# Performance work log

Hardware: AMD Instinct MI355X
Metric: run time of the kernel (lower is better)

Reference implementation:

```python
import jax, jax.numpy as jnp
import numpy as np

D_EMB = 1024
B, T = 8, 2048

def setup_inputs() -> dict:
    key = jax.random.key(0)
    ks = jax.random.split(key, 7)
    s = 0.02
    return {
        "x": jax.random.normal(ks[0], (B, T, D_EMB), dtype=jnp.float32),
        "W_attn": jax.random.normal(ks[1], (3 * D_EMB, D_EMB), dtype=jnp.float32) * s,
        "b_attn": jax.random.normal(ks[2], (3 * D_EMB,), dtype=jnp.float32) * s,
        "W_proj": jax.random.normal(ks[3], (D_EMB, D_EMB), dtype=jnp.float32) * s,
        "b_proj": jax.random.normal(ks[4], (D_EMB,), dtype=jnp.float32) * s,
        "W_fc": jax.random.normal(ks[5], (1, D_EMB), dtype=jnp.float32) * s,
        "b_fc": jax.random.normal(ks[6], (1,), dtype=jnp.float32) * s,
    }

def reference(x, W_attn, b_attn, W_proj, b_proj, W_fc, b_fc):
    # qkv projection: torch Linear => x @ W.T + b
    qkv = jnp.einsum('btc,dc->btd', x, W_attn) + b_attn          # [B,T,3C]
    q, k, v = jnp.split(qkv, 3, axis=2)                          # each [B,T,C]
    scale = q.shape[-1] ** (-0.5)
    attn_scores = jnp.einsum('btc,bsc->bts', q, k) * scale       # [B,T,T]
    attn_weights = jax.nn.softmax(attn_scores, axis=-1)          # traditional softmax
    y = jnp.einsum('bts,bsc->btc', attn_weights, v)              # [B,T,C]
    y = jnp.einsum('btc,dc->btd', y, W_proj) + b_proj            # [B,T,C]
    out = jnp.einsum('btc,oc->bto', y, W_fc) + b_fc              # [B,T,1]
    return out
```

## Files before the change

### kernel.cpp

```cpp
#include <hip/hip_runtime.h>
#include <stdint.h>

#define D_EMB 1024
#define NBATCH 8
#define SEQ 2048
#define MTOT (NBATCH*SEQ)

typedef __attribute__((ext_vector_type(8))) short short8;
typedef __attribute__((ext_vector_type(4))) float f32x4;

__device__ __forceinline__ ushort bf16r(float x) {
  union { float f; uint32_t u; } c; c.f = x;
  return (ushort)((c.u + 0x7fffu + ((c.u >> 16) & 1u)) >> 16);
}

__device__ __forceinline__ void cp16(const ushort* g, ushort* l) {
  __builtin_amdgcn_global_load_lds(
      (const __attribute__((address_space(1))) void*)g,
      (__attribute__((address_space(3))) void*)l, 16, 0, 0);
}

__global__ __launch_bounds__(256) void cvt_all(
    const float4* __restrict__ x4, const float4* __restrict__ W4,
    const float4* __restrict__ wv4, const float* __restrict__ sc,
    ushort* __restrict__ xb, ushort* __restrict__ wqkb, float* __restrict__ vw) {
  int tid = threadIdx.x;
  if (blockIdx.x < 4096) {
    int wave = tid >> 6, lane = tid & 63;
    long row = (long)blockIdx.x * 4 + wave;
    const float4* xr = x4 + row * 256;
    ushort* xo = xb + row * D_EMB;
    float s = 0.f;
    #pragma unroll
    for (int i = 0; i < 4; i++) {
      int idx = lane + i * 64;
      float4 v = xr[idx];
      float4 w = wv4[idx];
      *(ushort4*)(xo + idx * 4) = make_ushort4(bf16r(v.x), bf16r(v.y), bf16r(v.z), bf16r(v.w));
      s += v.x * w.x + v.y * w.y + v.z * w.z + v.w * w.w;
    }
    #pragma unroll
    for (int off = 32; off; off >>= 1) s += __shfl_xor(s, off);
    if (lane == 0) vw[row] = s + sc[1];
  } else {
    long base = (long)(blockIdx.x - 4096) * 1024 + tid;
    #pragma unroll
    for (int i = 0; i < 4; i++) {
      long idx = base + i * 256;
      float4 v = W4[idx];
      *(ushort4*)(wqkb + idx * 4) = make_ushort4(bf16r(v.x), bf16r(v.y), bf16r(v.z), bf16r(v.w));
    }
  }
}

__global__ void init_kernel(const float* __restrict__ bp, const float* __restrict__ Wfc,
                            const float* __restrict__ bfc,
                            float* __restrict__ w_eff, float* __restrict__ wv_eff,
                            float* __restrict__ numden, float* __restrict__ sc) {
  int tid = threadIdx.x;
  int b = blockIdx.x;
  if (b == 0) { w_eff[tid] = 0.f; return; }
  if (b == 1) { wv_eff[tid] = 0.f; return; }
  if (b >= 3) { numden[(long)(b - 3) * 1024 + tid] = 0.f; return; }
  float v = bp[tid] * Wfc[tid];
  int lane = tid & 63, w = tid >> 6;
  #pragma unroll
  for (int off = 32; off; off >>= 1) v += __shfl_xor(v, off);
  __shared__ float red[16];
  if (lane == 0) red[w] = v;
  __syncthreads();
  if (tid == 0) {
    float s = 0.f;
    #pragma unroll
    for (int i = 0; i < 16; i++) s += red[i];
    sc[0] = s + bfc[0];
  }
}

__global__ void prep1(const float* __restrict__ Wp, const float* __restrict__ Wfc,
                      float* __restrict__ w_eff) {
  int c = blockIdx.x * 256 + threadIdx.x;
  int d0 = blockIdx.y * 16;
  float s = 0.f;
  #pragma unroll
  for (int d = d0; d < d0 + 16; d++) s += Wfc[d] * Wp[(long)d * D_EMB + c];
  atomicAdd(&w_eff[c], s);
}

__global__ void prep2(const float* __restrict__ Wattn, const float* __restrict__ battn,
                      const float* __restrict__ w_eff, float* __restrict__ wv_eff,
                      float* __restrict__ sc) {
  int tid = threadIdx.x;
  if (blockIdx.y == 64) {
    if (blockIdx.x != 0) return;
    float v = 0.f;
    #pragma unroll
    for (int i = 0; i < 4; i++) { int c = tid + i * 256; v += battn[2048 + c] * w_eff[c]; }
    int lane = tid & 63, w = tid >> 6;
    #pragma unroll
    for (int off = 32; off; off >>= 1) v += __shfl_xor(v, off);
    __shared__ float red[4];
    if (lane == 0) red[w] = v;
    __syncthreads();
    if (tid == 0) sc[1] = red[0] + red[1] + red[2] + red[3];
    return;
  }
  int d = blockIdx.x * 256 + tid;
  int c0 = blockIdx.y * 16;
  float s = 0.f;
  #pragma unroll
  for (int c = c0; c < c0 + 16; c++) s += w_eff[c] * Wattn[(long)(2048 + c) * D_EMB + d];
  atomicAdd(&wv_eff[d], s);
}

template<bool FUSED, bool REMAP>
__global__ __launch_bounds__(512, 2) void gemm_nt(
    const ushort* __restrict__ A, long lda, long sAz,
    const ushort* __restrict__ B, long ldb, long sBz,
    ushort* __restrict__ C, long ldc,
    const float* __restrict__ bias, float scale, int K,
    const float* __restrict__ vw, float* __restrict__ num, float* __restrict__ den) {
  __shared__ __align__(16) ushort lds[65536];

  int bx, by, z;
  if (REMAP) {
    int f = (int)(blockIdx.x + 8u * blockIdx.y);
    int xcd = f & 7, g = f >> 3;
    bx = g & 7; by = xcd * 8 + (g >> 3); z = 0;
  } else {
    bx = blockIdx.x; by = blockIdx.y; z = blockIdx.z;
  }

  const ushort* Az = A + (long)z * sAz;
  const ushort* Bz = B + (long)z * sBz;
  long m0 = (long)by * 256, n0 = (long)bx * 256;
  int t = threadIdx.x;
  int wave = t >> 6, lane = t & 63;
  int r = lane & 15, q = lane >> 4;
  int wm = wave >> 2, wn = wave & 3;

  f32x4 acc[8][4] = {};

  int rl = t >> 3;
  int cs = t & 7;
  int gc = cs ^ (rl & 7);
  const ushort* pA = Az + (m0 + rl) * lda + gc * 8;
  const ushort* pB = Bz + (n0 + rl) * ldb + gc * 8;
  long a64 = 64 * lda, a128 = 128 * lda;
  long b64 = 64 * ldb, b128s = 128 * ldb;
  int dst = t * 8;

  int sw8 = (q ^ (r & 7)) * 8;
  int aoff = (wm * 128 + r) * 64 + sw8;
  int boff = (wn * 64 + r) * 64 + sw8;

  int NT = K >> 6;

#define STG_A(BUF, H, TT) do { \
    cp16(pA + (long)(TT) * 64 + (H) * a128,       lds + (BUF) * 16384 + (H) * 8192 + dst); \
    cp16(pA + (long)(TT) * 64 + (H) * a128 + a64, lds + (BUF) * 16384 + (H) * 8192 + 4096 + dst); \
  } while (0)
#define STG_B(BUF, H, TT) do { \
    cp16(pB + (long)(TT) * 64 + (H) * b128s,       lds + 32768 + (BUF) * 16384 + (H) * 8192 + dst); \
    cp16(pB + (long)(TT) * 64 + (H) * b128s + b64, lds + 32768 + (BUF) * 16384 + (H) * 8192 + 4096 + dst); \
  } while (0)

#define LDA_Q(BUF, QA) do { \
    _Pragma("unroll") \
    for (int i = 0; i < 4; i++) { \
      af[0][i] = *(const short8*)(lds + (BUF) * 16384 + ( aoff + (QA) * 4096 + i * 1024       )); \
      af[1][i] = *(const short8*)(lds + (BUF) * 16384 + ((aoff + (QA) * 4096 + i * 1024) ^ 32 )); \
    } \
  } while (0)
#define LDB_Q(BUF, QB, BF) do { \
    _Pragma("unroll") \
    for (int j = 0; j < 2; j++) { \
      BF[0][j] = *(const short8*)(lds + 32768 + (BUF) * 16384 + ( boff + (QB) * 2048 + j * 1024       )); \
      BF[1][j] = *(const short8*)(lds + 32768 + (BUF) * 16384 + ((boff + (QB) * 2048 + j * 1024) ^ 32 )); \
    } \
  } while (0)

#define MM_Q(QA, QB, BF) do { \
    __builtin_amdgcn_s_setprio(1); \
    _Pragma("unroll") \
    for (int kk = 0; kk < 2; kk++) { \
      _Pragma("unroll") \
      for (int i = 0; i < 4; i++) { \
        _Pragma("unroll") \
        for (int j = 0; j < 2; j++) \
          acc[(QA) * 4 + i][(QB) * 2 + j] = __builtin_amdgcn_mfma_f32_16x16x32_bf16( \
              af[kk][i], BF[kk][j], acc[(QA) * 4 + i][(QB) * 2 + j], 0, 0, 0); \
      } \
    } \
    __builtin_amdgcn_s_setprio(0); \
  } while (0)

#define BAR __builtin_amdgcn_s_barrier()
#define LGKM0 asm volatile("s_waitcnt lgkmcnt(0)" ::: "memory")
#define VM4 asm volatile("s_waitcnt vmcnt(4)" ::: "memory")
#define VM0 asm volatile("s_waitcnt vmcnt(0)" ::: "memory")

#define TILE(BUF, OB, TT, DOA, DOB, P4WAIT) do { \
    short8 af[2][4], bf0[2][2], bf1[2][2]; \
     \
    LDA_Q(BUF, 0); LDB_Q(BUF, 0, bf0); \
    if (DOA) STG_A(OB, 0, (TT) + 1); \
    BAR; LGKM0; MM_Q(0, 0, bf0); BAR; \
     \
    LDB_Q(BUF, 1, bf1); \
    if (DOA) STG_A(OB, 1, (TT) + 1); \
    BAR; LGKM0; MM_Q(0, 1, bf1); BAR; \
     \
    LDA_Q(BUF, 1); \
    if (DOB) STG_B(BUF, 0, (TT) + 2); \
    BAR; LGKM0; MM_Q(1, 1, bf1); BAR; \
     \
    if (DOB) STG_B(BUF, 1, (TT) + 2); \
    BAR; MM_Q(1, 0, bf0); P4WAIT; BAR; \
  } while (0)

  STG_A(0, 0, 0); STG_A(0, 1, 0); STG_B(0, 0, 0); STG_B(0, 1, 0);
  STG_B(1, 0, 1); STG_B(1, 1, 1);
  VM4;
  BAR;

  #pragma unroll 1
  for (int u = 0; u < NT - 2; u += 2) {
    TILE(0, 1, u,     true, true, VM4);
    TILE(1, 0, u + 1, true, true, VM4);
  }
  TILE(0, 1, NT - 2, true,  false, VM0);
  TILE(1, 0, NT - 1, false, false, (void)0);

#undef TILE
#undef BAR
#undef LGKM0
#undef VM4
#undef VM0
#undef MM_Q
#undef LDB_Q
#undef LDA_Q
#undef STG_B
#undef STG_A

  if (!FUSED) {
    #pragma unroll
    for (int fi = 0; fi < 8; fi++) {
      #pragma unroll
      for (int fj = 0; fj < 4; fj++) {
        long col = n0 + wn * 64 + fj * 16 + r;
        float bj = bias[col];
        #pragma unroll
        for (int rr = 0; rr < 4; rr++) {
          long row = m0 + wm * 128 + fi * 16 + q * 4 + rr;
          C[row * ldc + col] = bf16r(acc[fi][fj][rr] * scale + bj);
        }
      }
    }
  } else {
    const float* vwz = vw + (long)z * SEQ + n0;
    float* numz = num + (long)z * SEQ + m0;
    float* denz = den + (long)z * SEQ + m0;
    float vwj[4];
    #pragma unroll
    for (int fj = 0; fj < 4; fj++) vwj[fj] = vwz[wn * 64 + fj * 16 + r];
    #pragma unroll
    for (int fi = 0; fi < 8; fi++) {
      #pragma unroll
      for (int rr = 0; rr < 4; rr++) {
        float sn = 0.f, sd = 0.f;
        #pragma unroll
        for (int fj = 0; fj < 4; fj++) {
          float e = __expf(acc[fi][fj][rr] * scale);
          sd += e;
          sn += e * vwj[fj];
        }
        #pragma unroll
        for (int off = 1; off < 16; off <<= 1) {
          sn += __shfl_xor(sn, off);
          sd += __shfl_xor(sd, off);
        }
        if (r == 0) {
          int row = wm * 128 + fi * 16 + q * 4 + rr;
          atomicAdd(&numz[row], sn);
          atomicAdd(&denz[row], sd);
        }
      }
    }
  }
}

__global__ __launch_bounds__(256) void finalize(
    const float* __restrict__ num, const float* __restrict__ den,
    const float* __restrict__ sc, float* __restrict__ out) {
  long i = blockIdx.x * 256L + threadIdx.x;
  out[i] = num[i] / den[i] + sc[0];
}

extern "C" void kernel_launch(void* const* d_in, const int* in_sizes, int n_in,
                              void* d_out, int out_size, void* d_ws, size_t ws_size,
                              hipStream_t stream) {
  const float* x     = (const float*)d_in[0];
  const float* Wattn = (const float*)d_in[1];
  const float* battn = (const float*)d_in[2];
  const float* Wproj = (const float*)d_in[3];
  const float* bproj = (const float*)d_in[4];
  const float* Wfc   = (const float*)d_in[5];
  const float* bfc   = (const float*)d_in[6];
  float* out = (float*)d_out;

  const size_t OFF_XB    = 0;
  const size_t OFF_WQKB  = 33554432;
  const size_t OFF_QK    = 37748736;
  const size_t OFF_NUM   = 104857600;
  const size_t OFF_DEN   = 104923136;
  const size_t OFF_VW    = 104988672;
  const size_t OFF_WEFF  = 105054208;
  const size_t OFF_WVEFF = 105058304;
  const size_t OFF_SC    = 105062400;
  const size_t NEED      = 105062408;
  if (ws_size < NEED) return;

  char* ws = (char*)d_ws;
  ushort* xb    = (ushort*)(ws + OFF_XB);
  ushort* wqkb  = (ushort*)(ws + OFF_WQKB);
  ushort* qk    = (ushort*)(ws + OFF_QK);
  float* num    = (float*)(ws + OFF_NUM);
  float* den    = (float*)(ws + OFF_DEN);
  float* vw     = (float*)(ws + OFF_VW);
  float* w_eff  = (float*)(ws + OFF_WEFF);
  float* wv_eff = (float*)(ws + OFF_WVEFF);
  float* sc     = (float*)(ws + OFF_SC);

  init_kernel<<<dim3(35), dim3(1024), 0, stream>>>(bproj, Wfc, bfc, w_eff, wv_eff, num, sc);
  prep1<<<dim3(4, 64), dim3(256), 0, stream>>>(Wproj, Wfc, w_eff);
  prep2<<<dim3(4, 65), dim3(256), 0, stream>>>(Wattn, battn, w_eff, wv_eff, sc);

  cvt_all<<<dim3(4096 + 512), dim3(256), 0, stream>>>(
      (const float4*)x, (const float4*)Wattn, (const float4*)wv_eff, sc, xb, wqkb, vw);

  gemm_nt<false, true><<<dim3(8, 64, 1), dim3(512), 0, stream>>>(
      xb, (long)D_EMB, 0L, wqkb, (long)D_EMB, 0L,
      qk, 2048L, battn, 1.0f, D_EMB, nullptr, nullptr, nullptr);

  gemm_nt<true, false><<<dim3(8, 8, NBATCH), dim3(512), 0, stream>>>(
      qk, 2048L, (long)SEQ * 2048, qk + 1024, 2048L, (long)SEQ * 2048,
      nullptr, 0L, nullptr, 0.03125f, D_EMB, vw, num, den);

  finalize<<<dim3(64), dim3(256), 0, stream>>>(num, den, sc, out);
}
```

Baseline: 276.2 us.

## Make each GEMM block compute two M tiles sequentially with overlapped prologue

Each workgroup of both GEMMs now processes two consecutive 256-row M tiles, halving the grid to 256 blocks. The first tile's epilogue overlaps with the prefetch prologue for the second tile, and bias/vw loads are hoisted so they are fetched once per block. Block indices are remapped so batch/XCD assignment interleaves across the eight XCDs. The aim is to cut per-block launch/prologue cost and let epilogue stores overlap with loads. In exchange, the grid is smaller and may leave CUs idle. The prologue also writes LDS buffer 0 while other waves may still be reading it from the last tile.

```diff
diff --git a/kernel.cpp b/kernel.cpp
--- a/kernel.cpp
+++ b/kernel.cpp
@@ -113,7 +113,7 @@
   atomicAdd(&wv_eff[d], s);
 }
 
-template<bool FUSED, bool REMAP>
+template<bool FUSED>
 __global__ __launch_bounds__(512, 2) void gemm_nt(
     const ushort* __restrict__ A, long lda, long sAz,
     const ushort* __restrict__ B, long ldb, long sBz,
@@ -122,24 +122,34 @@
     const float* __restrict__ vw, float* __restrict__ num, float* __restrict__ den) {
   __shared__ __align__(16) ushort lds[65536];
 
-  int bx, by, z;
-  if (REMAP) {
-    int f = (int)(blockIdx.x + 8u * blockIdx.y);
+  int f = (int)blockIdx.x;
+  int bx, by0, z;
+  if (!FUSED) {
     int xcd = f & 7, g = f >> 3;
-    bx = g & 7; by = xcd * 8 + (g >> 3); z = 0;
+    bx = g & 7; by0 = xcd * 8 + (g >> 3) * 2; z = 0;
   } else {
-    bx = blockIdx.x; by = blockIdx.y; z = blockIdx.z;
+    z = f & 7; int g = f >> 3;
+    bx = g & 7; by0 = (g >> 3) * 2;
   }
 
   const ushort* Az = A + (long)z * sAz;
   const ushort* Bz = B + (long)z * sBz;
-  long m0 = (long)by * 256, n0 = (long)bx * 256;
+  long m0 = (long)by0 * 256, n0 = (long)bx * 256;
   int t = threadIdx.x;
   int wave = t >> 6, lane = t & 63;
   int r = lane & 15, q = lane >> 4;
   int wm = wave >> 2, wn = wave & 3;
 
   f32x4 acc[8][4] = {};
+
+  float bj4[4], vwj[4];
+  if (!FUSED) {
+    #pragma unroll
+    for (int fj = 0; fj < 4; fj++) bj4[fj] = bias[n0 + wn * 64 + fj * 16 + r];
+  } else {
+    #pragma unroll
+    for (int fj = 0; fj < 4; fj++) vwj[fj] = vw[(long)z * SEQ + n0 + wn * 64 + fj * 16 + r];
+  }
 
   int rl = t >> 3;
   int cs = t & 7;
@@ -219,19 +229,86 @@
     BAR; MM_Q(1, 0, bf0); P4WAIT; BAR; \
   } while (0)
 
-  STG_A(0, 0, 0); STG_A(0, 1, 0); STG_B(0, 0, 0); STG_B(0, 1, 0);
-  STG_B(1, 0, 1); STG_B(1, 1, 1);
+#define PROLOGUE do { \
+    STG_A(0, 0, 0); STG_A(0, 1, 0); STG_B(0, 0, 0); STG_B(0, 1, 0); \
+    STG_B(1, 0, 1); STG_B(1, 1, 1); \
+  } while (0)
+
+#define MAINLOOP do { \
+    _Pragma("unroll 1") \
+    for (int u = 0; u < NT - 2; u += 2) { \
+      TILE(0, 1, u,     true, true, VM4); \
+      TILE(1, 0, u + 1, true, true, VM4); \
+    } \
+    TILE(0, 1, NT - 2, true,  false, VM0); \
+    TILE(1, 0, NT - 1, false, false, (void)0); \
+  } while (0)
+
+#define EPILOGUE(M0) do { \
+    if (!FUSED) { \
+      _Pragma("unroll") \
+      for (int fi = 0; fi < 8; fi++) { \
+        _Pragma("unroll") \
+        for (int fj = 0; fj < 4; fj++) { \
+          long col = n0 + wn * 64 + fj * 16 + r; \
+          _Pragma("unroll") \
+          for (int rr = 0; rr < 4; rr++) { \
+            long row = (M0) + wm * 128 + fi * 16 + q * 4 + rr; \
+            C[row * ldc + col] = bf16r(acc[fi][fj][rr] * scale + bj4[fj]); \
+          } \
+        } \
+      } \
+    } else { \
+      float* numz = num + (long)z * SEQ + (M0); \
+      float* denz = den + (long)z * SEQ + (M0); \
+      _Pragma("unroll") \
+      for (int fi = 0; fi < 8; fi++) { \
+        _Pragma("unroll") \
+        for (int rr = 0; rr < 4; rr++) { \
+          float sn = 0.f, sd = 0.f; \
+          _Pragma("unroll") \
+          for (int fj = 0; fj < 4; fj++) { \
+            float e = __expf(acc[fi][fj][rr] * scale); \
+            sd += e; \
+            sn += e * vwj[fj]; \
+          } \
+          _Pragma("unroll") \
+          for (int off = 1; off < 16; off <<= 1) { \
+            sn += __shfl_xor(sn, off); \
+            sd += __shfl_xor(sd, off); \
+          } \
+          if (r == 0) { \
+            int row = wm * 128 + fi * 16 + q * 4 + rr; \
+            atomicAdd(&numz[row], sn); \
+            atomicAdd(&denz[row], sd); \
+          } \
+        } \
+      } \
+    } \
+  } while (0)
+
+  PROLOGUE;
   VM4;
   BAR;
-
-  #pragma unroll 1
-  for (int u = 0; u < NT - 2; u += 2) {
-    TILE(0, 1, u,     true, true, VM4);
-    TILE(1, 0, u + 1, true, true, VM4);
-  }
-  TILE(0, 1, NT - 2, true,  false, VM0);
-  TILE(1, 0, NT - 1, false, false, (void)0);
-
+  MAINLOOP;
+
+  pA += 256 * lda;
+  PROLOGUE;
+  EPILOGUE(m0);
+  #pragma unroll
+  for (int fi = 0; fi < 8; fi++)
+    #pragma unroll
+    for (int fj = 0; fj < 4; fj++)
+      acc[fi][fj] = (f32x4){0.f, 0.f, 0.f, 0.f};
+  VM4;
+  BAR;
+
+  MAINLOOP;
+  EPILOGUE(m0 + 256);
+
+#undef EPILOGUE
+#undef MAINLOOP
+#undef PROLOGUE
 #undef TILE
 #undef BAR
 #undef LGKM0
@@ -242,52 +319,6 @@
 #undef LDA_Q
 #undef STG_B
 #undef STG_A
-
-  if (!FUSED) {
-    #pragma unroll
-    for (int fi = 0; fi < 8; fi++) {
-      #pragma unroll
-      for (int fj = 0; fj < 4; fj++) {
-        long col = n0 + wn * 64 + fj * 16 + r;
-        float bj = bias[col];
-        #pragma unroll
-        for (int rr = 0; rr < 4; rr++) {
-          long row = m0 + wm * 128 + fi * 16 + q * 4 + rr;
-          C[row * ldc + col] = bf16r(acc[fi][fj][rr] * scale + bj);
-        }
-      }
-    }
-  } else {
-    const float* vwz = vw + (long)z * SEQ + n0;
-    float* numz = num + (long)z * SEQ + m0;
-    float* denz = den + (long)z * SEQ + m0;
-    float vwj[4];
-    #pragma unroll
-    for (int fj = 0; fj < 4; fj++) vwj[fj] = vwz[wn * 64 + fj * 16 + r];
-    #pragma unroll
-    for (int fi = 0; fi < 8; fi++) {
-      #pragma unroll
-      for (int rr = 0; rr < 4; rr++) {
-        float sn = 0.f, sd = 0.f;
-        #pragma unroll
-        for (int fj = 0; fj < 4; fj++) {
-          float e = __expf(acc[fi][fj][rr] * scale);
-          sd += e;
-          sn += e * vwj[fj];
-        }
-        #pragma unroll
-        for (int off = 1; off < 16; off <<= 1) {
-          sn += __shfl_xor(sn, off);
-          sd += __shfl_xor(sd, off);
-        }
-        if (r == 0) {
-          int row = wm * 128 + fi * 16 + q * 4 + rr;
-          atomicAdd(&numz[row], sn);
-          atomicAdd(&denz[row], sd);
-        }
-      }
-    }
-  }
 }
 
 __global__ __launch_bounds__(256) void finalize(
@@ -339,11 +370,11 @@
   cvt_all<<<dim3(4096 + 512), dim3(256), 0, stream>>>(
       (const float4*)x, (const float4*)Wattn, (const float4*)wv_eff, sc, xb, wqkb, vw);
 
-  gemm_nt<false, true><<<dim3(8, 64, 1), dim3(512), 0, stream>>>(
+  gemm_nt<false><<<dim3(256), dim3(512), 0, stream>>>(
       xb, (long)D_EMB, 0L, wqkb, (long)D_EMB, 0L,
       qk, 2048L, battn, 1.0f, D_EMB, nullptr, nullptr, nullptr);
 
-  gemm_nt<true, false><<<dim3(8, 8, NBATCH), dim3(512), 0, stream>>>(
+  gemm_nt<true><<<dim3(256), dim3(512), 0, stream>>>(
       qk, 2048L, (long)SEQ * 2048, qk + 1024, 2048L, (long)SEQ * 2048,
       nullptr, 0L, nullptr, 0.03125f, D_EMB, vw, num, den);
 
```

Result: slower. 290.7 us (+5.2%).
